# Performance work log

Hardware: AMD Instinct MI355X
Metric: run time of the kernel (lower is better)

The kernel has to match this reference:

```python
import jax, jax.numpy as jnp
import numpy as np

B, C, OUTC, H, W, K, P, S = 4, 64, 64, 128, 128, 3, 1, 1
KK = K * K


def setup_inputs() -> dict:
    key = jax.random.key(0)
    ks = jax.random.split(key, 5)
    x = jax.random.normal(ks[0], (B, C, H, W), dtype=jnp.float32)
    # small-scale offset weights keep learned offsets in a realistic few-pixel range
    w_off = jax.random.normal(ks[1], (2 * KK, C, 3, 3), dtype=jnp.float32) * 0.05
    b_off = jnp.zeros((2 * KK,), dtype=jnp.float32)
    w_mask = jax.random.normal(ks[2], (KK, C, 3, 3), dtype=jnp.float32) * 0.05
    b_mask = jnp.zeros((KK,), dtype=jnp.float32)
    w_dcn = jax.random.normal(ks[3], (OUTC, C, K, K), dtype=jnp.float32) * (1.0 / np.sqrt(C * KK))
    b_dcn = jnp.zeros((OUTC,), dtype=jnp.float32)
    return {"x": x, "w_off": w_off, "b_off": b_off, "w_mask": w_mask,
            "b_mask": b_mask, "w_dcn": w_dcn, "b_dcn": b_dcn}


def _conv3x3(x, w, b):
    y = jax.lax.conv_general_dilated(x, w, (1, 1), ((1, 1), (1, 1)),
                                     dimension_numbers=("NCHW", "OIHW", "NCHW"))
    return y + b[None, :, None, None]


def _deform_conv(x, offset, mask, w, b):
    # torchvision DeformConv2d (v2, modulated). offset layout: [B, kk, (dy,dx), H, W]
    Ho = (H + 2 * P - K) // S + 1
    Wo = (W + 2 * P - K) // S + 1
    off = offset.reshape(B, KK, 2, Ho, Wo)
    dy, dx = off[:, :, 0], off[:, :, 1]                      # [B,kk,Ho,Wo]
    ki, kj = jnp.meshgrid(jnp.arange(K), jnp.arange(K), indexing="ij")
    ki = ki.reshape(KK).astype(jnp.float32)
    kj = kj.reshape(KK).astype(jnp.float32)
    hg = (jnp.arange(Ho) * S - P).astype(jnp.float32)
    wg = (jnp.arange(Wo) * S - P).astype(jnp.float32)
    py = dy + ki[None, :, None, None] + hg[None, None, :, None]   # sample y coord
    px = dx + kj[None, :, None, None] + wg[None, None, None, :]   # sample x coord

    y0f = jnp.floor(py)
    x0f = jnp.floor(px)
    ly = py - y0f
    lx = px - x0f
    y0 = y0f.astype(jnp.int32)
    x0 = x0f.astype(jnp.int32)

    x_flat = x.reshape(B, C, H * W)

    def sample(yi, xi, wgt):
        valid = (yi >= 0) & (yi < H) & (xi >= 0) & (xi < W)
        idx = jnp.clip(yi, 0, H - 1) * W + jnp.clip(xi, 0, W - 1)  # [B,kk,Ho,Wo]
        g = jax.vmap(lambda xb, ib: xb[:, ib])(x_flat, idx)        # [B,C,kk,Ho,Wo]
        return g * (wgt * valid)[:, None]

    acc = (sample(y0, x0, (1 - ly) * (1 - lx))
           + sample(y0, x0 + 1, (1 - ly) * lx)
           + sample(y0 + 1, x0, ly * (1 - lx))
           + sample(y0 + 1, x0 + 1, ly * lx))                      # [B,C,kk,Ho,Wo]
    acc = acc * mask.reshape(B, 1, KK, Ho, Wo)
    out = jnp.einsum("bckhw,ock->bohw", acc, w.reshape(OUTC, C, KK))
    return out + b[None, :, None, None]


def reference(x, w_off, b_off, w_mask, b_mask, w_dcn, b_dcn):
    offset = _conv3x3(x, w_off, b_off)
    mask = jax.nn.sigmoid(_conv3x3(x, w_mask, b_mask))
    out = _deform_conv(x, offset, mask, w_dcn, b_dcn)
    return out, offset
```

## Files before the change

kernel.cpp:

```cpp
#include <hip/hip_runtime.h>
#include <hip/hip_bf16.h>
#include <math.h>

#define BB 4
#define CC 64
#define OCN 64
#define HH 128
#define WW 128
#define HW (HH*WW)
#define KKN 9
#define CK 576
#define APAD 200

typedef short short8 __attribute__((ext_vector_type(8)));
typedef float floatx4 __attribute__((ext_vector_type(4)));
typedef unsigned int uintx4 __attribute__((ext_vector_type(4)));

__device__ __forceinline__ float bf2f(__hip_bfloat16 h) {
    unsigned short u = *reinterpret_cast<unsigned short*>(&h);
    return __uint_as_float(((unsigned)u) << 16);
}
__device__ __forceinline__ short f2bfs(float f) {
    __hip_bfloat16 h = __float2bfloat16(f);
    return *reinterpret_cast<short*>(&h);
}
__device__ __forceinline__ uintx4 as_u4(short8 v) {
    union { short8 s; uintx4 u; } x; x.s = v; return x.u;
}
__device__ __forceinline__ float blo(unsigned d) { return __uint_as_float(d << 16); }
__device__ __forceinline__ float bhi(unsigned d) { return __uint_as_float(d & 0xffff0000u); }

__global__ __launch_bounds__(256) void transpose_prep(
    const float* __restrict__ x,
    const float* __restrict__ w_dcn, const float* __restrict__ w_off,
    const float* __restrict__ b_off, const float* __restrict__ w_mask,
    const float* __restrict__ b_mask,
    __hip_bfloat16* __restrict__ xt, __hip_bfloat16* __restrict__ wTf,
    __hip_bfloat16* __restrict__ wOf, float* __restrict__ rebias)
{
    int blk = blockIdx.x;
    int tid = threadIdx.x;
    if (blk < BB * 512) {
        __shared__ float tile[64][33];
        int pixbase = (blk & 511) * 32;
        int b       = blk >> 9;
        const float* xb = x + (size_t)b * CC * HW;
        int p = tid & 31;
        #pragma unroll
        for (int i = 0; i < 8; ++i) {
            int c = (tid >> 5) * 8 + i;
            tile[c][p] = xb[(size_t)c * HW + pixbase + p];
        }
        __syncthreads();
        __hip_bfloat16* xo = xt + ((size_t)b * HW + pixbase) * CC;
        int pixl = tid >> 3;
        int c8t  = tid & 7;
        short8 o;
        #pragma unroll
        for (int i = 0; i < 8; ++i) o[i] = f2bfs(tile[c8t * 8 + i][pixl]);
        *reinterpret_cast<short8*>(&xo[(size_t)pixl * CC + c8t * 8]) = o;
        return;
    }
    int i = (blk - BB * 512) * 256 + tid;
    if (i < 18 * 4 * 64 * 8) {
        int jj = i & 7;
        int l  = (i >> 3) & 63;
        int nt = (i >> 9) & 3;
        int s  = i >> 11;
        int oc = nt * 16 + (l & 15);
        int kk = s * 32 + ((l >> 4) << 3) + jj;
        int c  = kk & 63;
        int kt = kk >> 6;
        wTf[i] = __float2bfloat16(w_dcn[(oc * CC + c) * 9 + kt]);
    }
    int j = i - 18 * 4 * 64 * 8;
    if (j >= 0 && j < 18 * 2 * 64 * 8) {
        int jj = j & 7;
        int l  = (j >> 3) & 63;
        int nt = (j >> 9) & 1;
        int s  = j >> 10;
        int oc = nt * 16 + (l & 15);
        int kk = s * 32 + ((l >> 4) << 3) + jj;
        int c  = kk & 63;
        int kt = kk >> 6;
        float v = 0.0f;
        if (oc < 18)      v = w_off[(oc * CC + c) * 9 + kt];
        else if (oc < 27) v = w_mask[((oc - 18) * CC + c) * 9 + kt];
        wOf[j] = __float2bfloat16(v);
    }
    int r = j - 18 * 2 * 64 * 8;
    if (r >= 0 && r < 27) rebias[r] = (r < 18) ? b_off[r] : b_mask[r - 18];
}

__global__ __launch_bounds__(256, 8) void deform_fused(
    const __hip_bfloat16* __restrict__ xt,
    const __hip_bfloat16* __restrict__ wTf, const __hip_bfloat16* __restrict__ wOf,
    const float* __restrict__ rebias, const float* __restrict__ b_dcn,
    float* __restrict__ off_out, float* __restrict__ out)
{
    __shared__ __align__(16) __hip_bfloat16 accs[32][APAD];
    __shared__ uintx4 tabs[KKN][32];
    __shared__ float offs_l[18][33];
    __shared__ float ms_l[KKN][33];

    int tid  = threadIdx.x;
    int lane = tid & 63;
    int wv   = __builtin_amdgcn_readfirstlane(tid >> 6);
    int pix  = tid >> 3;
    int c8   = tid & 7;
    int spix = (tid >> 3) & 31;
    int nt   = wv & 1;
    int pg   = wv >> 1;

    int wo0 = (blockIdx.x & 3) * 32;
    int row = (blockIdx.x >> 2) & (HH - 1);
    int b   = blockIdx.x >> 9;

    const __hip_bfloat16* xtb16 = xt + (size_t)b * HW * CC;
    const short8 zero8 = {0,0,0,0,0,0,0,0};
    int kreg = (lane >> 4) << 3;

    floatx4 accom = {0, 0, 0, 0};
    for (int chunk = 0; chunk < 3; ++chunk) {
        int y = row + chunk - 1;
        bool yvalid = (unsigned)y < (unsigned)HH;
        short8 v[3];
        #pragma unroll
        for (int kl = 0; kl < 3; ++kl) {
            int xw = wo0 + spix + kl - 1;
            bool valid = yvalid && ((unsigned)xw < (unsigned)WW);
            v[kl] = zero8;
            if (valid)
                v[kl] = *reinterpret_cast<const short8*>(xtb16 + ((size_t)y * WW + xw) * CC + c8 * 8);
        }
        #pragma unroll
        for (int kl = 0; kl < 3; ++kl)
            *reinterpret_cast<short8*>(&accs[spix][kl * 64 + c8 * 8]) = v[kl];
        __syncthreads();

        #pragma unroll
        for (int step = 0; step < 6; ++step) {
            int s = chunk * 6 + step;
            short8 bfrag = *(reinterpret_cast<const short8*>(wOf) + (size_t)(s * 2 + nt) * 64 + lane);
            short8 a = *reinterpret_cast<const short8*>(&accs[pg * 16 + (lane & 15)][step * 32 + kreg]);
            accom = __builtin_amdgcn_mfma_f32_16x16x32_bf16(a, bfrag, accom, 0, 0, 0);
        }
        __syncthreads();
    }

    {
        int oc = nt * 16 + (lane & 15);
        int pcol = pg * 16 + ((lane >> 4) << 2);
        if (oc < 18) {
            float bias = rebias[oc];
            floatx4 o = accom;
            o[0] += bias; o[1] += bias; o[2] += bias; o[3] += bias;
            *reinterpret_cast<floatx4*>(&off_out[(((size_t)b * 18 + oc) * HH + row) * WW + wo0 + pcol]) = o;
            offs_l[oc][pcol]     = o[0];
            offs_l[oc][pcol + 1] = o[1];
            offs_l[oc][pcol + 2] = o[2];
            offs_l[oc][pcol + 3] = o[3];
        } else if (oc < 27) {
            float bias = rebias[oc];
            #pragma unroll
            for (int q = 0; q < 4; ++q)
                ms_l[oc - 18][pcol + q] = 1.0f / (1.0f + expf(-(accom[q] + bias)));
        }
    }
    __syncthreads();

    for (int e = tid; e < KKN * 32; e += 256) {
        int k = e >> 5, p = e & 31;
        float dy = offs_l[2 * k][p];
        float dx = offs_l[2 * k + 1][p];
        float m  = ms_l[k][p];
        float py = dy + (float)(k / 3) + (float)(row - 1);
        float px = dx + (float)(k % 3) + (float)(wo0 + p - 1);
        float y0f = floorf(py), x0f = floorf(px);
        float ly = py - y0f, lx = px - x0f;
        int y0 = (int)y0f, x0 = (int)x0f;
        uintx4 rec;
        #pragma unroll
        for (int t = 0; t < 4; ++t) {
            int yi = y0 + (t >> 1), xi = x0 + (t & 1);
            float wy = (t >> 1) ? ly : 1.0f - ly;
            float wx = (t & 1)  ? lx : 1.0f - lx;
            bool valid = ((unsigned)yi < (unsigned)HH) && ((unsigned)xi < (unsigned)WW);
            int yc = min(max(yi, 0), HH - 1);
            int xc = min(max(xi, 0), WW - 1);
            __hip_bfloat16 hw = __float2bfloat16(valid ? wy * wx * m : 0.0f);
            unsigned short wb = *reinterpret_cast<unsigned short*>(&hw);
            rec[t] = (unsigned)(yc * WW + xc) | ((unsigned)wb << 16);
        }
        tabs[k][p] = rec;
    }
    __syncthreads();

    const char* xtb = (const char*)xtb16;
    int co = c8 * 16;

    short8 buf[2][4];
    uintx4 tb[2];
    floatx4 accv[2] = {{0,0,0,0},{0,0,0,0}};

#define ISSUE(G9) do { \
    uintx4 _t = tabs[(G9)][pix]; \
    tb[(G9) & 1] = _t; \
    buf[(G9) & 1][0] = *(const short8*)(xtb + ((_t[0] & 0xffffu) << 7) + co); \
    buf[(G9) & 1][1] = *(const short8*)(xtb + ((_t[1] & 0xffffu) << 7) + co); \
    buf[(G9) & 1][2] = *(const short8*)(xtb + ((_t[2] & 0xffffu) << 7) + co); \
    buf[(G9) & 1][3] = *(const short8*)(xtb + ((_t[3] & 0xffffu) << 7) + co); \
} while (0)

#define COMBINE(G9) do { \
    float aA[8] = {0,0,0,0,0,0,0,0}; \
    _Pragma("unroll") \
    for (int t = 0; t < 4; ++t) { \
        float wt = __uint_as_float(tb[(G9) & 1][t] & 0xffff0000u); \
        uintx4 dA = as_u4(buf[(G9) & 1][t]); \
        _Pragma("unroll") \
        for (int jq = 0; jq < 4; ++jq) { \
            aA[2 * jq]     = fmaf(wt, blo(dA[jq]), aA[2 * jq]); \
            aA[2 * jq + 1] = fmaf(wt, bhi(dA[jq]), aA[2 * jq + 1]); \
        } \
    } \
    short8 oA; \
    _Pragma("unroll") \
    for (int jq = 0; jq < 8; ++jq) { oA[jq] = f2bfs(aA[jq]); } \
    *reinterpret_cast<short8*>(&accs[pix][((G9) % 3) * 64 + c8 * 8]) = oA; \
} while (0)

#define MFMA_CHUNK(CH) do { \
    _Pragma("unroll") \
    for (int step = 0; step < 6; ++step) { \
        int s = (CH) * 6 + step; \
        short8 bfrag = *(reinterpret_cast<const short8*>(wTf) + (size_t)(s * 4 + wv) * 64 + lane); \
        _Pragma("unroll") \
        for (int pgq = 0; pgq < 2; ++pgq) { \
            short8 a = *reinterpret_cast<const short8*>(&accs[pgq * 16 + (lane & 15)][step * 32 + kreg]); \
            accv[pgq] = __builtin_amdgcn_mfma_f32_16x16x32_bf16(a, bfrag, accv[pgq], 0, 0, 0); \
        } \
    } \
} while (0)

    ISSUE(0);
    ISSUE(1); COMBINE(0);
    ISSUE(2); COMBINE(1); COMBINE(2);
    __syncthreads();
    ISSUE(3);
    MFMA_CHUNK(0);
    asm volatile("s_waitcnt lgkmcnt(0)" ::: "memory");
    __builtin_amdgcn_s_barrier();
    ISSUE(4); COMBINE(3);
    ISSUE(5); COMBINE(4); COMBINE(5);
    __syncthreads();
    ISSUE(6);
    MFMA_CHUNK(1);
    asm volatile("s_waitcnt lgkmcnt(0)" ::: "memory");
    __builtin_amdgcn_s_barrier();
    ISSUE(7); COMBINE(6);
    ISSUE(8); COMBINE(7); COMBINE(8);
    __syncthreads();
    MFMA_CHUNK(2);

#undef ISSUE
#undef COMBINE
#undef MFMA_CHUNK

    int oc = wv * 16 + (lane & 15);
    float bias = b_dcn[oc];
    #pragma unroll
    for (int pgq = 0; pgq < 2; ++pgq) {
        int pcol = wo0 + pgq * 16 + ((lane >> 4) << 2);
        floatx4 o = accv[pgq];
        o[0] += bias; o[1] += bias; o[2] += bias; o[3] += bias;
        *reinterpret_cast<floatx4*>(&out[(((size_t)b * OCN + oc) * HH + row) * WW + pcol]) = o;
    }
}

extern "C" void kernel_launch(void* const* d_in, const int* in_sizes, int n_in,
                              void* d_out, int out_size, void* d_ws, size_t ws_size,
                              hipStream_t stream) {
    const float* x      = (const float*)d_in[0];
    const float* w_off  = (const float*)d_in[1];
    const float* b_off  = (const float*)d_in[2];
    const float* w_mask = (const float*)d_in[3];
    const float* b_mask = (const float*)d_in[4];
    const float* w_dcn  = (const float*)d_in[5];
    const float* b_dcn  = (const float*)d_in[6];

    float* out     = (float*)d_out;
    float* off_out = out + (size_t)BB * OCN * HW;

    float* rebias  = (float*)d_ws;
    __hip_bfloat16* xt  = (__hip_bfloat16*)(rebias + 32);
    __hip_bfloat16* wTf = xt + (size_t)BB * HW * CC;
    __hip_bfloat16* wOf = wTf + 18 * 4 * 64 * 8;

    int prep_total  = 18 * 4 * 64 * 8 + 18 * 2 * 64 * 8 + 27;
    int prep_blocks = (prep_total + 255) / 256;
    transpose_prep<<<BB * 512 + prep_blocks, 256, 0, stream>>>(
        x, w_dcn, w_off, b_off, w_mask, b_mask, xt, wTf, wOf, rebias);

    deform_fused<<<BB * HH * 4, 256, 0, stream>>>(
        xt, wTf, wOf, rebias, b_dcn, off_out, out);
}
```

Before: 41.61 us.

## Make each wavefront own 16 pixels end-to-end, removing block barriers

```diff
diff --git a/kernel.cpp b/kernel.cpp
--- a/kernel.cpp
+++ b/kernel.cpp
@@ -9,17 +9,11 @@
 #define WW 128
 #define HW (HH*WW)
 #define KKN 9
-#define CK 576
-#define APAD 200
 
 typedef short short8 __attribute__((ext_vector_type(8)));
 typedef float floatx4 __attribute__((ext_vector_type(4)));
 typedef unsigned int uintx4 __attribute__((ext_vector_type(4)));
 
-__device__ __forceinline__ float bf2f(__hip_bfloat16 h) {
-    unsigned short u = *reinterpret_cast<unsigned short*>(&h);
-    return __uint_as_float(((unsigned)u) << 16);
-}
 __device__ __forceinline__ short f2bfs(float f) {
     __hip_bfloat16 h = __float2bfloat16(f);
     return *reinterpret_cast<short*>(&h);
@@ -92,92 +86,136 @@
     if (r >= 0 && r < 27) rebias[r] = (r < 18) ? b_off[r] : b_mask[r - 18];
 }
 
-__global__ __launch_bounds__(256, 8) void deform_fused(
+#define SCR_OFF  0
+#define TABS_OFF 2592
+#define OFFS_OFF 4896
+#define MSL_OFF  6048
+#define WSTRIDE  6656
+
+__global__ __launch_bounds__(256, 4) void deform_fused(
     const __hip_bfloat16* __restrict__ xt,
     const __hip_bfloat16* __restrict__ wTf, const __hip_bfloat16* __restrict__ wOf,
     const float* __restrict__ rebias, const float* __restrict__ b_dcn,
     float* __restrict__ off_out, float* __restrict__ out)
 {
-    __shared__ __align__(16) __hip_bfloat16 accs[32][APAD];
-    __shared__ uintx4 tabs[KKN][32];
-    __shared__ float offs_l[18][33];
-    __shared__ float ms_l[KKN][33];
-
-    int tid  = threadIdx.x;
-    int lane = tid & 63;
-    int wv   = __builtin_amdgcn_readfirstlane(tid >> 6);
-    int pix  = tid >> 3;
-    int c8   = tid & 7;
-    int spix = (tid >> 3) & 31;
-    int nt   = wv & 1;
-    int pg   = wv >> 1;
-
-    int wo0 = (blockIdx.x & 3) * 32;
-    int row = (blockIdx.x >> 2) & (HH - 1);
-    int b   = blockIdx.x >> 9;
-
-    const __hip_bfloat16* xtb16 = xt + (size_t)b * HW * CC;
+    __shared__ __align__(16) char lds_all[4 * WSTRIDE];
+
+    int tid    = threadIdx.x;
+    int lane   = tid & 63;
+    int wv     = __builtin_amdgcn_readfirstlane(tid >> 6);
+    int lane15 = lane & 15;
+    int lq     = lane >> 4;
+    int px8    = lane >> 3;
+    int c8     = lane & 7;
+    int co     = c8 * 16;
+
+    int wo0  = (blockIdx.x & 1) * 64;
+    int row  = (blockIdx.x >> 1) & (HH - 1);
+    int b    = blockIdx.x >> 8;
+    int wcol = wo0 + wv * 16;
+
+    char*   wb    = lds_all + wv * WSTRIDE;
+    char*   scr_b = wb + SCR_OFF;
+    uintx4* tabsv = (uintx4*)(wb + TABS_OFF);
+    float*  offs  = (float*)(wb + OFFS_OFF);
+    float*  msl   = (float*)(wb + MSL_OFF);
+
+    const char* xtb = (const char*)(xt + (size_t)b * HW * CC);
+    const short8* wTf8 = (const short8*)wTf;
+    const short8* wOf8 = (const short8*)wOf;
     const short8 zero8 = {0,0,0,0,0,0,0,0};
-    int kreg = (lane >> 4) << 3;
-
-    floatx4 accom = {0, 0, 0, 0};
-    for (int chunk = 0; chunk < 3; ++chunk) {
-        int y = row + chunk - 1;
-        bool yvalid = (unsigned)y < (unsigned)HH;
-        short8 v[3];
-        #pragma unroll
-        for (int kl = 0; kl < 3; ++kl) {
-            int xw = wo0 + spix + kl - 1;
-            bool valid = yvalid && ((unsigned)xw < (unsigned)WW);
-            v[kl] = zero8;
-            if (valid)
-                v[kl] = *reinterpret_cast<const short8*>(xtb16 + ((size_t)y * WW + xw) * CC + c8 * 8);
+
+    floatx4 accom0 = {0,0,0,0}, accom1 = {0,0,0,0};
+
+#define ALOAD(KY, V0, V1, V2) do { \
+    int _y = row + (KY) - 1; \
+    bool _yv = (unsigned)_y < (unsigned)HH; \
+    int _yc = min(max(_y, 0), HH - 1); \
+    { int _xw = wcol + px8 - 1; \
+      bool _v = _yv && ((unsigned)_xw < (unsigned)WW); \
+      int _xc = min(max(_xw, 0), WW - 1); \
+      short8 _t = *(const short8*)(xtb + (((_yc * WW) + _xc) << 7) + co); \
+      V0 = _v ? _t : zero8; } \
+    { int _xw = wcol + px8 + 7; \
+      bool _v = _yv && ((unsigned)_xw < (unsigned)WW); \
+      int _xc = min(max(_xw, 0), WW - 1); \
+      short8 _t = *(const short8*)(xtb + (((_yc * WW) + _xc) << 7) + co); \
+      V1 = _v ? _t : zero8; } \
+    { int _xw = wcol + 16 + px8 - 1; \
+      bool _v = _yv && ((unsigned)_xw < (unsigned)WW); \
+      int _xc = min(max(_xw, 0), WW - 1); \
+      short8 _t = *(const short8*)(xtb + (((_yc * WW) + _xc) << 7) + co); \
+      V2 = _v ? _t : zero8; } \
+} while (0)
+
+#define ADSW(V0, V1, V2) do { \
+    *(short8*)(scr_b + px8 * 144 + co) = V0; \
+    *(short8*)(scr_b + (px8 + 8) * 144 + co) = V1; \
+    if (lane < 16) *(short8*)(scr_b + (16 + px8) * 144 + co) = V2; \
+} while (0)
+
+#define AMFMA(KY) do { \
+    _Pragma("unroll") \
+    for (int s6 = 0; s6 < 6; ++s6) { \
+        int kx = s6 >> 1; \
+        short8 a = *(const short8*)(scr_b + (lane15 + kx) * 144 + (s6 & 1) * 64 + lq * 16); \
+        const short8* bp = wOf8 + (size_t)(((KY) * 6 + s6) * 2) * 64 + lane; \
+        accom0 = __builtin_amdgcn_mfma_f32_16x16x32_bf16(a, bp[0],  accom0, 0, 0, 0); \
+        accom1 = __builtin_amdgcn_mfma_f32_16x16x32_bf16(a, bp[64], accom1, 0, 0, 0); \
+    } \
+} while (0)
+
+    {
+        short8 va0, va1, va2, vb0, vb1, vb2, vc0, vc1, vc2;
+        ALOAD(0, va0, va1, va2);
+        ADSW(va0, va1, va2);
+        ALOAD(1, vb0, vb1, vb2);
+        AMFMA(0);
+        ADSW(vb0, vb1, vb2);
+        ALOAD(2, vc0, vc1, vc2);
+        AMFMA(1);
+        ADSW(vc0, vc1, vc2);
+        AMFMA(2);
+    }
+#undef ALOAD
+#undef ADSW
+#undef AMFMA
+
+    {
+        float bias0 = rebias[lane15];
+        floatx4 o0 = accom0;
+        o0[0] += bias0; o0[1] += bias0; o0[2] += bias0; o0[3] += bias0;
+        *reinterpret_cast<floatx4*>(
+            &off_out[(((size_t)b * 18 + lane15) * HH + row) * WW + wcol + lq * 4]) = o0;
+        ((floatx4*)offs)[lane15 * 4 + lq] = o0;
+        int bi = min(16 + lane15, 26);
+        float bias1 = rebias[bi];
+        if (lane15 < 2) {
+            floatx4 o1 = accom1;
+            o1[0] += bias1; o1[1] += bias1; o1[2] += bias1; o1[3] += bias1;
+            *reinterpret_cast<floatx4*>(
+                &off_out[(((size_t)b * 18 + 16 + lane15) * HH + row) * WW + wcol + lq * 4]) = o1;
+            ((floatx4*)offs)[(16 + lane15) * 4 + lq] = o1;
+        } else if (lane15 < 11) {
+            floatx4 m;
+            #pragma unroll
+            for (int q = 0; q < 4; ++q) m[q] = 1.0f / (1.0f + expf(-(accom1[q] + bias1)));
+            ((floatx4*)msl)[(lane15 - 2) * 4 + lq] = m;
         }
-        #pragma unroll
-        for (int kl = 0; kl < 3; ++kl)
-            *reinterpret_cast<short8*>(&accs[spix][kl * 64 + c8 * 8]) = v[kl];
-        __syncthreads();
-
-        #pragma unroll
-        for (int step = 0; step < 6; ++step) {
-            int s = chunk * 6 + step;
-            short8 bfrag = *(reinterpret_cast<const short8*>(wOf) + (size_t)(s * 2 + nt) * 64 + lane);
-            short8 a = *reinterpret_cast<const short8*>(&accs[pg * 16 + (lane & 15)][step * 32 + kreg]);
-            accom = __builtin_amdgcn_mfma_f32_16x16x32_bf16(a, bfrag, accom, 0, 0, 0);
-        }
-        __syncthreads();
-    }
-
-    {
-        int oc = nt * 16 + (lane & 15);
-        int pcol = pg * 16 + ((lane >> 4) << 2);
-        if (oc < 18) {
-            float bias = rebias[oc];
-            floatx4 o = accom;
-            o[0] += bias; o[1] += bias; o[2] += bias; o[3] += bias;
-            *reinterpret_cast<floatx4*>(&off_out[(((size_t)b * 18 + oc) * HH + row) * WW + wo0 + pcol]) = o;
-            offs_l[oc][pcol]     = o[0];
-            offs_l[oc][pcol + 1] = o[1];
-            offs_l[oc][pcol + 2] = o[2];
-            offs_l[oc][pcol + 3] = o[3];
-        } else if (oc < 27) {
-            float bias = rebias[oc];
-            #pragma unroll
-            for (int q = 0; q < 4; ++q)
-                ms_l[oc - 18][pcol + q] = 1.0f / (1.0f + expf(-(accom[q] + bias)));
-        }
-    }
-    __syncthreads();
-
-    for (int e = tid; e < KKN * 32; e += 256) {
-        int k = e >> 5, p = e & 31;
-        float dy = offs_l[2 * k][p];
-        float dx = offs_l[2 * k + 1][p];
-        float m  = ms_l[k][p];
+    }
+
+    #pragma unroll
+    for (int r = 0; r < 3; ++r) {
+        int e = lane + r * 64;
+        if (r == 2 && lane >= 16) break;
+        int k = e >> 4, p = e & 15;
+        float dy = offs[(2 * k) * 16 + p];
+        float dx = offs[(2 * k + 1) * 16 + p];
+        float m  = msl[k * 16 + p];
         float py = dy + (float)(k / 3) + (float)(row - 1);
-        float px = dx + (float)(k % 3) + (float)(wo0 + p - 1);
-        float y0f = floorf(py), x0f = floorf(px);
-        float ly = py - y0f, lx = px - x0f;
+        float px_ = dx + (float)(k % 3) + (float)(wcol + p - 1);
+        float y0f = floorf(py), x0f = floorf(px_);
+        float ly = py - y0f, lx = px_ - x0f;
         int y0 = (int)y0f, x0 = (int)x0f;
         uintx4 rec;
         #pragma unroll
@@ -189,92 +227,110 @@
             int yc = min(max(yi, 0), HH - 1);
             int xc = min(max(xi, 0), WW - 1);
             __hip_bfloat16 hw = __float2bfloat16(valid ? wy * wx * m : 0.0f);
-            unsigned short wb = *reinterpret_cast<unsigned short*>(&hw);
-            rec[t] = (unsigned)(yc * WW + xc) | ((unsigned)wb << 16);
+            unsigned short wbb = *reinterpret_cast<unsigned short*>(&hw);
+            rec[t] = (unsigned)(yc * WW + xc) | ((unsigned)wbb << 16);
         }
-        tabs[k][p] = rec;
-    }
-    __syncthreads();
-
-    const char* xtb = (const char*)xtb16;
-    int co = c8 * 16;
-
-    short8 buf[2][4];
-    uintx4 tb[2];
-    floatx4 accv[2] = {{0,0,0,0},{0,0,0,0}};
-
-#define ISSUE(G9) do { \
-    uintx4 _t = tabs[(G9)][pix]; \
-    tb[(G9) & 1] = _t; \
-    buf[(G9) & 1][0] = *(const short8*)(xtb + ((_t[0] & 0xffffu) << 7) + co); \
-    buf[(G9) & 1][1] = *(const short8*)(xtb + ((_t[1] & 0xffffu) << 7) + co); \
-    buf[(G9) & 1][2] = *(const short8*)(xtb + ((_t[2] & 0xffffu) << 7) + co); \
-    buf[(G9) & 1][3] = *(const short8*)(xtb + ((_t[3] & 0xffffu) << 7) + co); \
-} while (0)
-
-#define COMBINE(G9) do { \
-    float aA[8] = {0,0,0,0,0,0,0,0}; \
-    _Pragma("unroll") \
-    for (int t = 0; t < 4; ++t) { \
-        float wt = __uint_as_float(tb[(G9) & 1][t] & 0xffff0000u); \
-        uintx4 dA = as_u4(buf[(G9) & 1][t]); \
-        _Pragma("unroll") \
-        for (int jq = 0; jq < 4; ++jq) { \
-            aA[2 * jq]     = fmaf(wt, blo(dA[jq]), aA[2 * jq]); \
-            aA[2 * jq + 1] = fmaf(wt, bhi(dA[jq]), aA[2 * jq + 1]); \
-        } \
-    } \
-    short8 oA; \
-    _Pragma("unroll") \
-    for (int jq = 0; jq < 8; ++jq) { oA[jq] = f2bfs(aA[jq]); } \
-    *reinterpret_cast<short8*>(&accs[pix][((G9) % 3) * 64 + c8 * 8]) = oA; \
-} while (0)
-
-#define MFMA_CHUNK(CH) do { \
-    _Pragma("unroll") \
-    for (int step = 0; step < 6; ++step) { \
-        int s = (CH) * 6 + step; \
-        short8 bfrag = *(reinterpret_cast<const short8*>(wTf) + (size_t)(s * 4 + wv) * 64 + lane); \
-        _Pragma("unroll") \
-        for (int pgq = 0; pgq < 2; ++pgq) { \
-            short8 a = *reinterpret_cast<const short8*>(&accs[pgq * 16 + (lane & 15)][step * 32 + kreg]); \
-            accv[pgq] = __builtin_amdgcn_mfma_f32_16x16x32_bf16(a, bfrag, accv[pgq], 0, 0, 0); \
-        } \
-    } \
-} while (0)
-
-    ISSUE(0);
-    ISSUE(1); COMBINE(0);
-    ISSUE(2); COMBINE(1); COMBINE(2);
-    __syncthreads();
-    ISSUE(3);
-    MFMA_CHUNK(0);
-    asm volatile("s_waitcnt lgkmcnt(0)" ::: "memory");
-    __builtin_amdgcn_s_barrier();
-    ISSUE(4); COMBINE(3);
-    ISSUE(5); COMBINE(4); COMBINE(5);
-    __syncthreads();
-    ISSUE(6);
-    MFMA_CHUNK(1);
-    asm volatile("s_waitcnt lgkmcnt(0)" ::: "memory");
-    __builtin_amdgcn_s_barrier();
-    ISSUE(7); COMBINE(6);
-    ISSUE(8); COMBINE(7); COMBINE(8);
-    __syncthreads();
-    MFMA_CHUNK(2);
-
-#undef ISSUE
-#undef COMBINE
-#undef MFMA_CHUNK
-
-    int oc = wv * 16 + (lane & 15);
-    float bias = b_dcn[oc];
-    #pragma unroll
-    for (int pgq = 0; pgq < 2; ++pgq) {
-        int pcol = wo0 + pgq * 16 + ((lane >> 4) << 2);
-        floatx4 o = accv[pgq];
-        o[0] += bias; o[1] += bias; o[2] += bias; o[3] += bias;
-        *reinterpret_cast<floatx4*>(&out[(((size_t)b * OCN + oc) * HH + row) * WW + pcol]) = o;
+        tabsv[k * 16 + p] = rec;
+    }
+
+    floatx4 accv0 = {0,0,0,0}, accv1 = {0,0,0,0}, accv2 = {0,0,0,0}, accv3 = {0,0,0,0};
+
+#define CLOAD(K, P0,P1,P2,P3, Q0,Q1,Q2,Q3) do { \
+    uintx4 _ua = tabsv[(K) * 16 + px8]; \
+    uintx4 _ub = tabsv[(K) * 16 + px8 + 8]; \
+    P0 = *(const short8*)(xtb + ((_ua[0] & 0xffffu) << 7) + co); \
+    P1 = *(const short8*)(xtb + ((_ua[1] & 0xffffu) << 7) + co); \
+    P2 = *(const short8*)(xtb + ((_ua[2] & 0xffffu) << 7) + co); \
+    P3 = *(const short8*)(xtb + ((_ua[3] & 0xffffu) << 7) + co); \
+    Q0 = *(const short8*)(xtb + ((_ub[0] & 0xffffu) << 7) + co); \
+    Q1 = *(const short8*)(xtb + ((_ub[1] & 0xffffu) << 7) + co); \
+    Q2 = *(const short8*)(xtb + ((_ub[2] & 0xffffu) << 7) + co); \
+    Q3 = *(const short8*)(xtb + ((_ub[3] & 0xffffu) << 7) + co); \
+} while (0)
+
+#define CCOMB(K, P0,P1,P2,P3, Q0,Q1,Q2,Q3) do { \
+    uintx4 _ua = tabsv[(K) * 16 + px8]; \
+    uintx4 _ub = tabsv[(K) * 16 + px8 + 8]; \
+    float fA[8] = {0,0,0,0,0,0,0,0}; \
+    float fB[8] = {0,0,0,0,0,0,0,0}; \
+    { float w = __uint_as_float(_ua[0] & 0xffff0000u); uintx4 d = as_u4(P0); \
+      _Pragma("unroll") for (int jq = 0; jq < 4; ++jq) { \
+        fA[2*jq] = fmaf(w, blo(d[jq]), fA[2*jq]); fA[2*jq+1] = fmaf(w, bhi(d[jq]), fA[2*jq+1]); } } \
+    { float w = __uint_as_float(_ua[1] & 0xffff0000u); uintx4 d = as_u4(P1); \
+      _Pragma("unroll") for (int jq = 0; jq < 4; ++jq) { \
+        fA[2*jq] = fmaf(w, blo(d[jq]), fA[2*jq]); fA[2*jq+1] = fmaf(w, bhi(d[jq]), fA[2*jq+1]); } } \
+    { float w = __uint_as_float(_ua[2] & 0xffff0000u); uintx4 d = as_u4(P2); \
+      _Pragma("unroll") for (int jq = 0; jq < 4; ++jq) { \
+        fA[2*jq] = fmaf(w, blo(d[jq]), fA[2*jq]); fA[2*jq+1] = fmaf(w, bhi(d[jq]), fA[2*jq+1]); } } \
+    { float w = __uint_as_float(_ua[3] & 0xffff0000u); uintx4 d = as_u4(P3); \
+      _Pragma("unroll") for (int jq = 0; jq < 4; ++jq) { \
+        fA[2*jq] = fmaf(w, blo(d[jq]), fA[2*jq]); fA[2*jq+1] = fmaf(w, bhi(d[jq]), fA[2*jq+1]); } } \
+    { float w = __uint_as_float(_ub[0] & 0xffff0000u); uintx4 d = as_u4(Q0); \
+      _Pragma("unroll") for (int jq = 0; jq < 4; ++jq) { \
+        fB[2*jq] = fmaf(w, blo(d[jq]), fB[2*jq]); fB[2*jq+1] = fmaf(w, bhi(d[jq]), fB[2*jq+1]); } } \
+    { float w = __uint_as_float(_ub[1] & 0xffff0000u); uintx4 d = as_u4(Q1); \
+      _Pragma("unroll") for (int jq = 0; jq < 4; ++jq) { \
+        fB[2*jq] = fmaf(w, blo(d[jq]), fB[2*jq]); fB[2*jq+1] = fmaf(w, bhi(d[jq]), fB[2*jq+1]); } } \
+    { float w = __uint_as_float(_ub[2] & 0xffff0000u); uintx4 d = as_u4(Q2); \
+      _Pragma("unroll") for (int jq = 0; jq < 4; ++jq) { \
+        fB[2*jq] = fmaf(w, blo(d[jq]), fB[2*jq]); fB[2*jq+1] = fmaf(w, bhi(d[jq]), fB[2*jq+1]); } } \
+    { float w = __uint_as_float(_ub[3] & 0xffff0000u); uintx4 d = as_u4(Q3); \
+      _Pragma("unroll") for (int jq = 0; jq < 4; ++jq) { \
+        fB[2*jq] = fmaf(w, blo(d[jq]), fB[2*jq]); fB[2*jq+1] = fmaf(w, bhi(d[jq]), fB[2*jq+1]); } } \
+    short8 oA, oB; \
+    _Pragma("unroll") for (int jq = 0; jq < 8; ++jq) { oA[jq] = f2bfs(fA[jq]); oB[jq] = f2bfs(fB[jq]); } \
+    *(short8*)(scr_b + px8 * 144 + co) = oA; \
+    *(short8*)(scr_b + (px8 + 8) * 144 + co) = oB; \
+} while (0)
+
+#define CMFMA(K) do { \
+    short8 a0 = *(const short8*)(scr_b + lane15 * 144 + lq * 16); \
+    short8 a1 = *(const short8*)(scr_b + lane15 * 144 + 64 + lq * 16); \
+    const short8* bp = wTf8 + (size_t)(8 * (K)) * 64 + lane; \
+    accv0 = __builtin_amdgcn_mfma_f32_16x16x32_bf16(a0, bp[0],   accv0, 0, 0, 0); \
+    accv1 = __builtin_amdgcn_mfma_f32_16x16x32_bf16(a0, bp[64],  accv1, 0, 0, 0); \
+    accv2 = __builtin_amdgcn_mfma_f32_16x16x32_bf16(a0, bp[128], accv2, 0, 0, 0); \
+    accv3 = __builtin_amdgcn_mfma_f32_16x16x32_bf16(a0, bp[192], accv3, 0, 0, 0); \
+    accv0 = __builtin_amdgcn_mfma_f32_16x16x32_bf16(a1, bp[256], accv0, 0, 0, 0); \
+    accv1 = __builtin_amdgcn_mfma_f32_16x16x32_bf16(a1, bp[320], accv1, 0, 0, 0); \
+    accv2 = __builtin_amdgcn_mfma_f32_16x16x32_bf16(a1, bp[384], accv2, 0, 0, 0); \
+    accv3 = __builtin_amdgcn_mfma_f32_16x16x32_bf16(a1, bp[448], accv3, 0, 0, 0); \
+} while (0)
+
+    {
+        short8 xa0, xa1, xa2, xa3, xb0, xb1, xb2, xb3;
+        short8 ya0, ya1, ya2, ya3, yb0, yb1, yb2, yb3;
+        CLOAD(0, xa0,xa1,xa2,xa3, xb0,xb1,xb2,xb3);
+        CLOAD(1, ya0,ya1,ya2,ya3, yb0,yb1,yb2,yb3);
+        CCOMB(0, xa0,xa1,xa2,xa3, xb0,xb1,xb2,xb3); CLOAD(2, xa0,xa1,xa2,xa3, xb0,xb1,xb2,xb3); CMFMA(0);
+        CCOMB(1, ya0,ya1,ya2,ya3, yb0,yb1,yb2,yb3); CLOAD(3, ya0,ya1,ya2,ya3, yb0,yb1,yb2,yb3); CMFMA(1);
+        CCOMB(2, xa0,xa1,xa2,xa3, xb0,xb1,xb2,xb3); CLOAD(4, xa0,xa1,xa2,xa3, xb0,xb1,xb2,xb3); CMFMA(2);
+        CCOMB(3, ya0,ya1,ya2,ya3, yb0,yb1,yb2,yb3); CLOAD(5, ya0,ya1,ya2,ya3, yb0,yb1,yb2,yb3); CMFMA(3);
+        CCOMB(4, xa0,xa1,xa2,xa3, xb0,xb1,xb2,xb3); CLOAD(6, xa0,xa1,xa2,xa3, xb0,xb1,xb2,xb3); CMFMA(4);
+        CCOMB(5, ya0,ya1,ya2,ya3, yb0,yb1,yb2,yb3); CLOAD(7, ya0,ya1,ya2,ya3, yb0,yb1,yb2,yb3); CMFMA(5);
+        CCOMB(6, xa0,xa1,xa2,xa3, xb0,xb1,xb2,xb3); CLOAD(8, xa0,xa1,xa2,xa3, xb0,xb1,xb2,xb3); CMFMA(6);
+        CCOMB(7, ya0,ya1,ya2,ya3, yb0,yb1,yb2,yb3);                                             CMFMA(7);
+        CCOMB(8, xa0,xa1,xa2,xa3, xb0,xb1,xb2,xb3);                                             CMFMA(8);
+    }
+#undef CLOAD
+#undef CCOMB
+#undef CMFMA
+
+    {
+        int pcol = wcol + lq * 4;
+        float bias;
+        bias = b_dcn[lane15];
+        accv0[0] += bias; accv0[1] += bias; accv0[2] += bias; accv0[3] += bias;
+        *reinterpret_cast<floatx4*>(&out[(((size_t)b * OCN + lane15) * HH + row) * WW + pcol]) = accv0;
+        bias = b_dcn[16 + lane15];
+        accv1[0] += bias; accv1[1] += bias; accv1[2] += bias; accv1[3] += bias;
+        *reinterpret_cast<floatx4*>(&out[(((size_t)b * OCN + 16 + lane15) * HH + row) * WW + pcol]) = accv1;
+        bias = b_dcn[32 + lane15];
+        accv2[0] += bias; accv2[1] += bias; accv2[2] += bias; accv2[3] += bias;
+        *reinterpret_cast<floatx4*>(&out[(((size_t)b * OCN + 32 + lane15) * HH + row) * WW + pcol]) = accv2;
+        bias = b_dcn[48 + lane15];
+        accv3[0] += bias; accv3[1] += bias; accv3[2] += bias; accv3[3] += bias;
+        *reinterpret_cast<floatx4*>(&out[(((size_t)b * OCN + 48 + lane15) * HH + row) * WW + pcol]) = accv3;
     }
 }
 
@@ -302,6 +358,6 @@
     transpose_prep<<<BB * 512 + prep_blocks, 256, 0, stream>>>(
         x, w_dcn, w_off, b_off, w_mask, b_mask, xt, wTf, wOf, rebias);
 
-    deform_fused<<<BB * HH * 4, 256, 0, stream>>>(
+    deform_fused<<<BB * HH * 2, 256, 0, stream>>>(
         xt, wTf, wOf, rebias, b_dcn, off_out, out);
 }
```

Result: slower. 46.55 us (+11.9%).

## Widen deform tile to 64 pixels per block to amortize weight loads

Applied to the files above, without the earlier changes.

```diff
diff --git a/kernel.cpp b/kernel.cpp
--- a/kernel.cpp
+++ b/kernel.cpp
@@ -9,15 +9,14 @@
 #define WW 128
 #define HW (HH*WW)
 #define KKN 9
-#define CK 576
 #define APAD 200
 
 typedef short short8 __attribute__((ext_vector_type(8)));
+typedef short short4v __attribute__((ext_vector_type(4)));
 typedef float floatx4 __attribute__((ext_vector_type(4)));
 typedef unsigned int uintx4 __attribute__((ext_vector_type(4)));
 
-__device__ __forceinline__ float bf2f(__hip_bfloat16 h) {
-    unsigned short u = *reinterpret_cast<unsigned short*>(&h);
+__device__ __forceinline__ float bf2f_us(unsigned short u) {
     return __uint_as_float(((unsigned)u) << 16);
 }
 __device__ __forceinline__ short f2bfs(float f) {
@@ -92,88 +91,105 @@
     if (r >= 0 && r < 27) rebias[r] = (r < 18) ? b_off[r] : b_mask[r - 18];
 }
 
-__global__ __launch_bounds__(256, 8) void deform_fused(
+__global__ __launch_bounds__(256, 4) void deform_fused(
     const __hip_bfloat16* __restrict__ xt,
     const __hip_bfloat16* __restrict__ wTf, const __hip_bfloat16* __restrict__ wOf,
     const float* __restrict__ rebias, const float* __restrict__ b_dcn,
     float* __restrict__ off_out, float* __restrict__ out)
 {
-    __shared__ __align__(16) __hip_bfloat16 accs[32][APAD];
-    __shared__ uintx4 tabs[KKN][32];
-    __shared__ float offs_l[18][33];
-    __shared__ float ms_l[KKN][33];
-
-    int tid  = threadIdx.x;
-    int lane = tid & 63;
-    int wv   = __builtin_amdgcn_readfirstlane(tid >> 6);
-    int pix  = tid >> 3;
-    int c8   = tid & 7;
-    int spix = (tid >> 3) & 31;
-    int nt   = wv & 1;
-    int pg   = wv >> 1;
-
-    int wo0 = (blockIdx.x & 3) * 32;
-    int row = (blockIdx.x >> 2) & (HH - 1);
-    int b   = blockIdx.x >> 9;
-
-    const __hip_bfloat16* xtb16 = xt + (size_t)b * HW * CC;
+    __shared__ __align__(16) __hip_bfloat16 accs[64][APAD];
+    __shared__ uintx4 tabs[KKN][64];
+    __shared__ __hip_bfloat16 offs_l[18][68];
+    __shared__ __hip_bfloat16 ms_l[KKN][68];
+
+    int tid    = threadIdx.x;
+    int lane   = tid & 63;
+    int wv     = __builtin_amdgcn_readfirstlane(tid >> 6);
+    int lane15 = lane & 15;
+    int lq     = lane >> 4;
+    int nt     = wv & 1;
+    int ph     = wv >> 1;
+    int pix    = tid >> 3;
+    int c8     = tid & 7;
+    int co     = c8 * 16;
+    int kreg   = lq << 3;
+
+    int wo0 = (blockIdx.x & 1) * 64;
+    int row = (blockIdx.x >> 1) & (HH - 1);
+    int b   = blockIdx.x >> 8;
+
+    const char* xtb = (const char*)(xt + (size_t)b * HW * CC);
+    const short8* wTf8 = (const short8*)wTf;
+    const short8* wOf8 = (const short8*)wOf;
     const short8 zero8 = {0,0,0,0,0,0,0,0};
-    int kreg = (lane >> 4) << 3;
-
-    floatx4 accom = {0, 0, 0, 0};
+
+    floatx4 accomA[2] = {{0,0,0,0},{0,0,0,0}};
     for (int chunk = 0; chunk < 3; ++chunk) {
         int y = row + chunk - 1;
         bool yvalid = (unsigned)y < (unsigned)HH;
-        short8 v[3];
-        #pragma unroll
-        for (int kl = 0; kl < 3; ++kl) {
-            int xw = wo0 + spix + kl - 1;
-            bool valid = yvalid && ((unsigned)xw < (unsigned)WW);
-            v[kl] = zero8;
-            if (valid)
-                v[kl] = *reinterpret_cast<const short8*>(xtb16 + ((size_t)y * WW + xw) * CC + c8 * 8);
-        }
-        #pragma unroll
-        for (int kl = 0; kl < 3; ++kl)
-            *reinterpret_cast<short8*>(&accs[spix][kl * 64 + c8 * 8]) = v[kl];
+        int yc = min(max(y, 0), HH - 1);
+        short8 v[2][3];
+        #pragma unroll
+        for (int h = 0; h < 2; ++h) {
+            #pragma unroll
+            for (int kl = 0; kl < 3; ++kl) {
+                int xw = wo0 + h * 32 + pix + kl - 1;
+                bool valid = yvalid && ((unsigned)xw < (unsigned)WW);
+                int xc = min(max(xw, 0), WW - 1);
+                short8 t = *(const short8*)(xtb + (((yc * WW) + xc) << 7) + co);
+                v[h][kl] = valid ? t : zero8;
+            }
+        }
+        #pragma unroll
+        for (int h = 0; h < 2; ++h)
+            #pragma unroll
+            for (int kl = 0; kl < 3; ++kl)
+                *reinterpret_cast<short8*>(&accs[h * 32 + pix][kl * 64 + c8 * 8]) = v[h][kl];
         __syncthreads();
 
         #pragma unroll
         for (int step = 0; step < 6; ++step) {
             int s = chunk * 6 + step;
-            short8 bfrag = *(reinterpret_cast<const short8*>(wOf) + (size_t)(s * 2 + nt) * 64 + lane);
-            short8 a = *reinterpret_cast<const short8*>(&accs[pg * 16 + (lane & 15)][step * 32 + kreg]);
-            accom = __builtin_amdgcn_mfma_f32_16x16x32_bf16(a, bfrag, accom, 0, 0, 0);
+            short8 bfrag = wOf8[(size_t)(s * 2 + nt) * 64 + lane];
+            #pragma unroll
+            for (int q = 0; q < 2; ++q) {
+                int pg = ph * 2 + q;
+                short8 a = *reinterpret_cast<const short8*>(&accs[pg * 16 + lane15][step * 32 + kreg]);
+                accomA[q] = __builtin_amdgcn_mfma_f32_16x16x32_bf16(a, bfrag, accomA[q], 0, 0, 0);
+            }
         }
         __syncthreads();
     }
 
-    {
-        int oc = nt * 16 + (lane & 15);
-        int pcol = pg * 16 + ((lane >> 4) << 2);
+    #pragma unroll
+    for (int q = 0; q < 2; ++q) {
+        int pg = ph * 2 + q;
+        int pcl = pg * 16 + lq * 4;
+        int oc = nt * 16 + lane15;
         if (oc < 18) {
             float bias = rebias[oc];
-            floatx4 o = accom;
+            floatx4 o = accomA[q];
             o[0] += bias; o[1] += bias; o[2] += bias; o[3] += bias;
-            *reinterpret_cast<floatx4*>(&off_out[(((size_t)b * 18 + oc) * HH + row) * WW + wo0 + pcol]) = o;
-            offs_l[oc][pcol]     = o[0];
-            offs_l[oc][pcol + 1] = o[1];
-            offs_l[oc][pcol + 2] = o[2];
-            offs_l[oc][pcol + 3] = o[3];
+            *reinterpret_cast<floatx4*>(
+                &off_out[(((size_t)b * 18 + oc) * HH + row) * WW + wo0 + pcl]) = o;
+            short4v ob = { f2bfs(o[0]), f2bfs(o[1]), f2bfs(o[2]), f2bfs(o[3]) };
+            *reinterpret_cast<short4v*>(&offs_l[oc][pcl]) = ob;
         } else if (oc < 27) {
             float bias = rebias[oc];
+            short4v mb;
             #pragma unroll
-            for (int q = 0; q < 4; ++q)
-                ms_l[oc - 18][pcol + q] = 1.0f / (1.0f + expf(-(accom[q] + bias)));
-        }
-    }
-    __syncthreads();
-
-    for (int e = tid; e < KKN * 32; e += 256) {
-        int k = e >> 5, p = e & 31;
-        float dy = offs_l[2 * k][p];
-        float dx = offs_l[2 * k + 1][p];
-        float m  = ms_l[k][p];
+            for (int t = 0; t < 4; ++t)
+                mb[t] = f2bfs(1.0f / (1.0f + expf(-(accomA[q][t] + bias))));
+            *reinterpret_cast<short4v*>(&ms_l[oc - 18][pcl]) = mb;
+        }
+    }
+    __syncthreads();
+
+    for (int e = tid; e < KKN * 64; e += 256) {
+        int k = e >> 6, p = e & 63;
+        float dy = bf2f_us(*(const unsigned short*)&offs_l[2 * k][p]);
+        float dx = bf2f_us(*(const unsigned short*)&offs_l[2 * k + 1][p]);
+        float m  = bf2f_us(*(const unsigned short*)&ms_l[k][p]);
         float py = dy + (float)(k / 3) + (float)(row - 1);
         float px = dx + (float)(k % 3) + (float)(wo0 + p - 1);
         float y0f = floorf(py), x0f = floorf(px);
@@ -186,95 +202,104 @@
             float wy = (t >> 1) ? ly : 1.0f - ly;
             float wx = (t & 1)  ? lx : 1.0f - lx;
             bool valid = ((unsigned)yi < (unsigned)HH) && ((unsigned)xi < (unsigned)WW);
-            int yc = min(max(yi, 0), HH - 1);
-            int xc = min(max(xi, 0), WW - 1);
+            int yc2 = min(max(yi, 0), HH - 1);
+            int xc2 = min(max(xi, 0), WW - 1);
             __hip_bfloat16 hw = __float2bfloat16(valid ? wy * wx * m : 0.0f);
             unsigned short wb = *reinterpret_cast<unsigned short*>(&hw);
-            rec[t] = (unsigned)(yc * WW + xc) | ((unsigned)wb << 16);
+            rec[t] = (unsigned)(yc2 * WW + xc2) | ((unsigned)wb << 16);
         }
         tabs[k][p] = rec;
     }
     __syncthreads();
-
-    const char* xtb = (const char*)xtb16;
-    int co = c8 * 16;
 
     short8 buf[2][4];
     uintx4 tb[2];
-    floatx4 accv[2] = {{0,0,0,0},{0,0,0,0}};
-
-#define ISSUE(G9) do { \
-    uintx4 _t = tabs[(G9)][pix]; \
-    tb[(G9) & 1] = _t; \
-    buf[(G9) & 1][0] = *(const short8*)(xtb + ((_t[0] & 0xffffu) << 7) + co); \
-    buf[(G9) & 1][1] = *(const short8*)(xtb + ((_t[1] & 0xffffu) << 7) + co); \
-    buf[(G9) & 1][2] = *(const short8*)(xtb + ((_t[2] & 0xffffu) << 7) + co); \
-    buf[(G9) & 1][3] = *(const short8*)(xtb + ((_t[3] & 0xffffu) << 7) + co); \
+    floatx4 accv[4] = {{0,0,0,0},{0,0,0,0},{0,0,0,0},{0,0,0,0}};
+
+#define ISSUE(G) do { \
+    uintx4 _t = tabs[(G) >> 1][pix + ((G) & 1) * 32]; \
+    tb[(G) & 1] = _t; \
+    buf[(G) & 1][0] = *(const short8*)(xtb + ((_t[0] & 0xffffu) << 7) + co); \
+    buf[(G) & 1][1] = *(const short8*)(xtb + ((_t[1] & 0xffffu) << 7) + co); \
+    buf[(G) & 1][2] = *(const short8*)(xtb + ((_t[2] & 0xffffu) << 7) + co); \
+    buf[(G) & 1][3] = *(const short8*)(xtb + ((_t[3] & 0xffffu) << 7) + co); \
 } while (0)
 
-#define COMBINE(G9) do { \
-    float aA[8] = {0,0,0,0,0,0,0,0}; \
+#define COMBINE(G) do { \
+    float fA[8] = {0,0,0,0,0,0,0,0}; \
     _Pragma("unroll") \
     for (int t = 0; t < 4; ++t) { \
-        float wt = __uint_as_float(tb[(G9) & 1][t] & 0xffff0000u); \
-        uintx4 dA = as_u4(buf[(G9) & 1][t]); \
+        float wt = __uint_as_float(tb[(G) & 1][t] & 0xffff0000u); \
+        uintx4 dA = as_u4(buf[(G) & 1][t]); \
         _Pragma("unroll") \
         for (int jq = 0; jq < 4; ++jq) { \
-            aA[2 * jq]     = fmaf(wt, blo(dA[jq]), aA[2 * jq]); \
-            aA[2 * jq + 1] = fmaf(wt, bhi(dA[jq]), aA[2 * jq + 1]); \
+            fA[2 * jq]     = fmaf(wt, blo(dA[jq]), fA[2 * jq]); \
+            fA[2 * jq + 1] = fmaf(wt, bhi(dA[jq]), fA[2 * jq + 1]); \
         } \
     } \
     short8 oA; \
     _Pragma("unroll") \
-    for (int jq = 0; jq < 8; ++jq) { oA[jq] = f2bfs(aA[jq]); } \
-    *reinterpret_cast<short8*>(&accs[pix][((G9) % 3) * 64 + c8 * 8]) = oA; \
+    for (int jq = 0; jq < 8; ++jq) { oA[jq] = f2bfs(fA[jq]); } \
+    *reinterpret_cast<short8*>( \
+        &accs[((G) & 1) * 32 + pix][(((G) >> 1) % 3) * 64 + c8 * 8]) = oA; \
 } while (0)
 
-#define MFMA_CHUNK(CH) do { \
+#define CMFMA(CH) do { \
     _Pragma("unroll") \
     for (int step = 0; step < 6; ++step) { \
         int s = (CH) * 6 + step; \
-        short8 bfrag = *(reinterpret_cast<const short8*>(wTf) + (size_t)(s * 4 + wv) * 64 + lane); \
+        short8 bfrag = wTf8[(size_t)(s * 4 + wv) * 64 + lane]; \
         _Pragma("unroll") \
-        for (int pgq = 0; pgq < 2; ++pgq) { \
-            short8 a = *reinterpret_cast<const short8*>(&accs[pgq * 16 + (lane & 15)][step * 32 + kreg]); \
-            accv[pgq] = __builtin_amdgcn_mfma_f32_16x16x32_bf16(a, bfrag, accv[pgq], 0, 0, 0); \
+        for (int pg = 0; pg < 4; ++pg) { \
+            short8 a = *reinterpret_cast<const short8*>(&accs[pg * 16 + lane15][step * 32 + kreg]); \
+            accv[pg] = __builtin_amdgcn_mfma_f32_16x16x32_bf16(a, bfrag, accv[pg], 0, 0, 0); \
         } \
     } \
 } while (0)
 
-    ISSUE(0);
-    ISSUE(1); COMBINE(0);
-    ISSUE(2); COMBINE(1); COMBINE(2);
-    __syncthreads();
-    ISSUE(3);
-    MFMA_CHUNK(0);
+    ISSUE(0); ISSUE(1);
+    COMBINE(0); ISSUE(2);
+    COMBINE(1); ISSUE(3);
+    COMBINE(2); ISSUE(4);
+    COMBINE(3); ISSUE(5);
+    COMBINE(4); COMBINE(5);
+    __syncthreads();
+    ISSUE(6); ISSUE(7);
+    CMFMA(0);
     asm volatile("s_waitcnt lgkmcnt(0)" ::: "memory");
     __builtin_amdgcn_s_barrier();
-    ISSUE(4); COMBINE(3);
-    ISSUE(5); COMBINE(4); COMBINE(5);
-    __syncthreads();
-    ISSUE(6);
-    MFMA_CHUNK(1);
+    COMBINE(6); ISSUE(8);
+    COMBINE(7); ISSUE(9);
+    COMBINE(8); ISSUE(10);
+    COMBINE(9); ISSUE(11);
+    COMBINE(10); COMBINE(11);
+    __syncthreads();
+    ISSUE(12); ISSUE(13);
+    CMFMA(1);
     asm volatile("s_waitcnt lgkmcnt(0)" ::: "memory");
     __builtin_amdgcn_s_barrier();
-    ISSUE(7); COMBINE(6);
-    ISSUE(8); COMBINE(7); COMBINE(8);
-    __syncthreads();
-    MFMA_CHUNK(2);
+    COMBINE(12); ISSUE(14);
+    COMBINE(13); ISSUE(15);
+    COMBINE(14); ISSUE(16);
+    COMBINE(15); ISSUE(17);
+    COMBINE(16); COMBINE(17);
+    __syncthreads();
+    CMFMA(2);
 
 #undef ISSUE
 #undef COMBINE
-#undef MFMA_CHUNK
-
-    int oc = wv * 16 + (lane & 15);
-    float bias = b_dcn[oc];
-    #pragma unroll
-    for (int pgq = 0; pgq < 2; ++pgq) {
-        int pcol = wo0 + pgq * 16 + ((lane >> 4) << 2);
-        floatx4 o = accv[pgq];
-        o[0] += bias; o[1] += bias; o[2] += bias; o[3] += bias;
-        *reinterpret_cast<floatx4*>(&out[(((size_t)b * OCN + oc) * HH + row) * WW + pcol]) = o;
+#undef CMFMA
+
+    {
+        int oc = wv * 16 + lane15;
+        float bias = b_dcn[oc];
+        #pragma unroll
+        for (int pg = 0; pg < 4; ++pg) {
+            int pcol = wo0 + pg * 16 + lq * 4;
+            floatx4 o = accv[pg];
+            o[0] += bias; o[1] += bias; o[2] += bias; o[3] += bias;
+            *reinterpret_cast<floatx4*>(&out[(((size_t)b * OCN + oc) * HH + row) * WW + pcol]) = o;
+        }
     }
 }
 
@@ -302,6 +327,6 @@
     transpose_prep<<<BB * 512 + prep_blocks, 256, 0, stream>>>(
         x, w_dcn, w_off, b_off, w_mask, b_mask, xt, wTf, wOf, rebias);
 
-    deform_fused<<<BB * HH * 4, 256, 0, stream>>>(
+    deform_fused<<<BB * HH * 2, 256, 0, stream>>>(
         xt, wTf, wOf, rebias, b_dcn, off_out, out);
 }
```

New measurement: 39.96 us. 1.04x faster.
